# Optimization experiments

Hardware: AMD Instinct MI355X
Metric: run time of the kernel (lower is better)

Reference implementation:

```python
import jax, jax.numpy as jnp
import numpy as np

N = 100000   # neuron_count (nodes)
D = 128      # node feature dim
E = 2000000  # edges
NW = 8       # number of distinct weight matrices


def setup_inputs() -> dict:
    key = jax.random.key(0)
    k1, k2, k3, k4, k5 = jax.random.split(key, 5)
    x = jax.random.normal(k1, (N, D), dtype=jnp.float32)
    W = jax.random.normal(k2, (NW, D, D), dtype=jnp.float32) * 0.02
    u = jax.random.randint(k3, (E,), 0, N)      # edge source nodes
    v = jax.random.randint(k4, (E,), 0, N)      # edge dest nodes
    widx = jax.random.randint(k5, (E,), 0, NW)  # per-edge weight index
    return {"x": x, "W": W, "u": u, "v": v, "widx": widx}


def reference(x, W, u, v, widx):
    # DGL update_all: per-edge message m_e = W[widx_e] @ x[u_e], then
    # x_out[v] = tanh(sum of incoming m). Because the message is linear in
    # x_src, we aggregate source features per (weight-index, dest-node)
    # segment first, then apply each weight matrix once (grouped GEMM):
    #   out[v, i] = tanh( sum_w sum_j W[w, i, j] * S[w, v, j] )
    seg = widx * N + v                                   # combined segment id
    S = jax.ops.segment_sum(x[u], seg, num_segments=NW * N)  # [NW*N, D]
    S = S.reshape(NW, N, D)
    out = jnp.einsum("wij,wvj->vi", W, S)                # [N, D]
    # zero in-degree nodes: DGL gives 0 feature; tanh(0)=0, consistent.
    return jnp.tanh(out)
```

## Files before the change

### kernel.cpp

```cpp
#include <hip/hip_runtime.h>
#include <math.h>

#define D 128

typedef __attribute__((ext_vector_type(8))) short bf8;
typedef __attribute__((ext_vector_type(4))) float f32x4;

__device__ __forceinline__ unsigned short f2bf_rne(float f) {
  unsigned u = __float_as_uint(f);
  unsigned r = (u + 0x7FFFu + ((u >> 16) & 1u)) >> 16;
  return (unsigned short)r;
}
__device__ __forceinline__ float bf2f(unsigned short h) {
  return __uint_as_float(((unsigned)h) << 16);
}
__device__ __forceinline__ float bflo(unsigned p) {
  return __uint_as_float(p << 16);
}
__device__ __forceinline__ float bfhi(unsigned p) {
  return __uint_as_float(p & 0xFFFF0000u);
}

__global__ __launch_bounds__(256) void prep_kernel(
    const float* __restrict__ x, unsigned short* __restrict__ xbf,
    long long xTotal, int xcGrid,
    const int* __restrict__ v, const int* __restrict__ widx,
    int* __restrict__ cnt2, int* __restrict__ rank,
    long long E, long long N) {
  if (blockIdx.x < (unsigned)xcGrid) {
    long long i0 = ((long long)blockIdx.x * 256 + threadIdx.x) * 8;
    if (i0 + 8 > xTotal) return;
    float4 f0 = *(const float4*)(x + i0);
    float4 f1 = *(const float4*)(x + i0 + 4);
    unsigned short o[8];
    o[0] = f2bf_rne(f0.x); o[1] = f2bf_rne(f0.y);
    o[2] = f2bf_rne(f0.z); o[3] = f2bf_rne(f0.w);
    o[4] = f2bf_rne(f1.x); o[5] = f2bf_rne(f1.y);
    o[6] = f2bf_rne(f1.z); o[7] = f2bf_rne(f1.w);
    *(bf8*)(xbf + i0) = *(bf8*)o;
  } else {
    long long base = (long long)(blockIdx.x - xcGrid) * 1024;
    #pragma unroll
    for (int k = 0; k < 4; ++k) {
      long long e = base + k * 256 + threadIdx.x;
      if (e < E) {
        long long seg = (long long)widx[e] * N + v[e];
        rank[e] = atomicAdd(&cnt2[seg], 1);
      }
    }
  }
}

__global__ __launch_bounds__(1024) void scanA_kernel(
    const int* __restrict__ cnt2, int* __restrict__ starts2,
    int* __restrict__ blkSums, long long NB2) {
  __shared__ int part[1024];
  int tid = threadIdx.x;
  long long base = (long long)blockIdx.x * 4096 + tid * 4;
  int c[4];
  #pragma unroll
  for (int i = 0; i < 4; ++i)
    c[i] = (base + i < NB2) ? cnt2[base + i] : 0;
  int loc[4];
  int sum = 0;
  #pragma unroll
  for (int i = 0; i < 4; ++i) { loc[i] = sum; sum += c[i]; }
  part[tid] = sum;
  __syncthreads();
  for (int off = 1; off < 1024; off <<= 1) {
    int val = (tid >= off) ? part[tid - off] : 0;
    __syncthreads();
    part[tid] += val;
    __syncthreads();
  }
  int excl = (tid == 0) ? 0 : part[tid - 1];
  #pragma unroll
  for (int i = 0; i < 4; ++i)
    if (base + i < NB2) starts2[base + i] = excl + loc[i];
  if (tid == 1023) blkSums[blockIdx.x] = part[1023];
}

__global__ __launch_bounds__(1024) void scanC_kernel(
    int* __restrict__ starts2, const int* __restrict__ blkSums,
    long long NB2, int Etot, int nBlk) {
  __shared__ int part[256];
  int tid = threadIdx.x;
  if (tid < 256) part[tid] = (tid < nBlk) ? blkSums[tid] : 0;
  __syncthreads();
  for (int off = 1; off < 256; off <<= 1) {
    int val = 0;
    if (tid < 256 && tid >= off) val = part[tid - off];
    __syncthreads();
    if (tid < 256) part[tid] += val;
    __syncthreads();
  }
  int off = (blockIdx.x == 0) ? 0 : part[blockIdx.x - 1];
  long long base = (long long)blockIdx.x * 4096 + tid * 4;
  #pragma unroll
  for (int i = 0; i < 4; ++i) {
    long long idx = base + i;
    if (idx < NB2) starts2[idx] += off;
  }
  if (blockIdx.x == 0 && tid == 0) starts2[NB2] = Etot;
}

__global__ __launch_bounds__(256) void scatwc_kernel(
    const float* __restrict__ W, unsigned short* __restrict__ Wp, int NW,
    int wpGrid,
    const int* __restrict__ u, const int* __restrict__ v,
    const int* __restrict__ widx, const int* __restrict__ rank,
    const int* __restrict__ starts2, int* __restrict__ sortedU,
    long long E, long long N) {
  if (blockIdx.x < (unsigned)wpGrid) {
    int idx = blockIdx.x * 256 + threadIdx.x;
    if (idx >= NW * 2048) return;
    int lane = idx & 63;
    int ks = (idx >> 6) & 3;
    int n  = (idx >> 8) & 7;
    int w  = idx >> 11;
    int row = n * 16 + (lane & 15);
    int col = ks * 32 + (lane >> 4) * 8;
    const float* src = W + (size_t)w * D * D + (size_t)row * D + col;
    unsigned short hi[8], re[8];
    #pragma unroll
    for (int e = 0; e < 8; ++e) {
      float f = src[e];
      unsigned short h = f2bf_rne(f);
      hi[e] = h;
      re[e] = f2bf_rne(f - bf2f(h));
    }
    int frag = (w * 8 + n) * 4 + ks;
    unsigned short* dst = Wp + (size_t)frag * 1024 + lane * 8;
    *(bf8*)dst = *(bf8*)hi;
    *(bf8*)(dst + 512) = *(bf8*)re;
  } else {
    long long base = (long long)(blockIdx.x - wpGrid) * 1024;
    #pragma unroll
    for (int k = 0; k < 4; ++k) {
      long long e = base + k * 256 + threadIdx.x;
      if (e < E) {
        long long seg = (long long)widx[e] * N + v[e];
        int pos = starts2[seg] + rank[e];
        sortedU[pos] = u[e] * 32;
      }
    }
  }
}

__global__ __launch_bounds__(256) void gather_pack_kernel(
    const unsigned short* __restrict__ xbf, const int* __restrict__ starts2,
    const int* __restrict__ sortedU, unsigned short* __restrict__ Sp,
    long long N, long long nt16) {
  __shared__ float T[16][132];
  int tid = threadIdx.x;
  long long w = blockIdx.y;
  long long rt = blockIdx.x;
  long long r0 = rt * 16;
  int grp = tid >> 5;
  int lane = tid & 31;

  #pragma unroll
  for (int rr = 0; rr < 2; ++rr) {
    int rloc = grp + rr * 8;
    long long r = r0 + rloc;
    float ax = 0.f, ay = 0.f, az = 0.f, aw = 0.f;
    if (r < N) {
      long long seg = w * N + r;
      int s0 = starts2[seg];
      int s1 = starts2[seg + 1];
      const uint2* xb = (const uint2*)xbf;
      int i = s0;
      for (; i + 4 <= s1; i += 4) {
        int u0 = sortedU[i], u1 = sortedU[i + 1];
        int u2 = sortedU[i + 2], u3 = sortedU[i + 3];
        uint2 a0 = xb[(size_t)u0 + lane];
        uint2 a1 = xb[(size_t)u1 + lane];
        uint2 a2 = xb[(size_t)u2 + lane];
        uint2 a3 = xb[(size_t)u3 + lane];
        ax += (bflo(a0.x) + bflo(a1.x)) + (bflo(a2.x) + bflo(a3.x));
        ay += (bfhi(a0.x) + bfhi(a1.x)) + (bfhi(a2.x) + bfhi(a3.x));
        az += (bflo(a0.y) + bflo(a1.y)) + (bflo(a2.y) + bflo(a3.y));
        aw += (bfhi(a0.y) + bfhi(a1.y)) + (bfhi(a2.y) + bfhi(a3.y));
      }
      for (; i < s1; ++i) {
        int uu = sortedU[i];
        uint2 a = xb[(size_t)uu + lane];
        ax += bflo(a.x); ay += bfhi(a.x);
        az += bflo(a.y); aw += bfhi(a.y);
      }
    }
    *(float4*)&T[rloc][lane * 4] = make_float4(ax, ay, az, aw);
  }
  __syncthreads();

  int ks = tid >> 6;
  int l = tid & 63;
  const float* src = &T[l & 15][ks * 32 + (l >> 4) * 8];
  unsigned short o[8];
  #pragma unroll
  for (int e = 0; e < 8; ++e) o[e] = f2bf_rne(src[e]);
  size_t frag = ((size_t)w * nt16 + rt) * 4 + ks;
  *(bf8*)(Sp + frag * 512 + (size_t)l * 8) = *(bf8*)o;
}

template<int NWT>
__global__ __launch_bounds__(256, 3) void mfma_gemm_kernel(
    const unsigned short* __restrict__ Sp, const unsigned short* __restrict__ Wp,
    float* __restrict__ out, long long N, long long nt16, int NWdyn) {
  int tid = threadIdx.x;
  int wv = tid >> 6;
  int wr = wv >> 1;
  int wc = wv & 1;
  int l = tid & 63;
  long long rtBase = (long long)blockIdx.x * 4 + wr * 2;

  const unsigned short* SA = Sp + (size_t)rtBase * 2048 + (size_t)l * 8;
  const unsigned short* WB = Wp + (size_t)wc * 16384 + (size_t)l * 8;
  const size_t wStrideS = (size_t)nt16 * 2048;

  f32x4 acc[2][4];
  #pragma unroll
  for (int m = 0; m < 2; ++m)
    #pragma unroll
    for (int n = 0; n < 4; ++n) acc[m][n] = (f32x4)(0.f);

  if (NWT == 8) {
    bf8 a[4][2], bh[2][4], br[2][4];
    {
      a[0][0] = *(const bf8*)(SA);
      a[0][1] = *(const bf8*)(SA + 2048);
      a[1][0] = *(const bf8*)(SA + 512);
      a[1][1] = *(const bf8*)(SA + 512 + 2048);
      a[2][0] = *(const bf8*)(SA + 1024);
      a[2][1] = *(const bf8*)(SA + 1024 + 2048);
      #pragma unroll
      for (int n = 0; n < 4; ++n) {
        bh[0][n] = *(const bf8*)(WB + n * 4096);
        br[0][n] = *(const bf8*)(WB + n * 4096 + 512);
      }
    }
    #pragma unroll
    for (int s = 0; s < 32; ++s) {
      const int abuf = s & 3;
      const int bbuf = s & 1;
      if (s + 3 < 32) {
        const int t = s + 3, w2 = t >> 2, ks2 = t & 3;
        const unsigned short* sa = SA + (size_t)w2 * wStrideS + ks2 * 512;
        a[(s + 3) & 3][0] = *(const bf8*)(sa);
        a[(s + 3) & 3][1] = *(const bf8*)(sa + 2048);
      }
      if (s + 1 < 32) {
        const int t = s + 1, w2 = t >> 2, ks2 = t & 3;
        const unsigned short* wb = WB + (size_t)w2 * 32768 + ks2 * 1024;
        #pragma unroll
        for (int n = 0; n < 4; ++n) {
          bh[bbuf ^ 1][n] = *(const bf8*)(wb + n * 4096);
          br[bbuf ^ 1][n] = *(const bf8*)(wb + n * 4096 + 512);
        }
      }
      #pragma unroll
      for (int n = 0; n < 4; ++n)
        #pragma unroll
        for (int m = 0; m < 2; ++m) {
          acc[m][n] = __builtin_amdgcn_mfma_f32_16x16x32_bf16(a[abuf][m], bh[bbuf][n], acc[m][n], 0, 0, 0);
          acc[m][n] = __builtin_amdgcn_mfma_f32_16x16x32_bf16(a[abuf][m], br[bbuf][n], acc[m][n], 0, 0, 0);
        }
    }
  } else {
    for (int w = 0; w < NWdyn; ++w) {
      #pragma unroll
      for (int ks = 0; ks < 4; ++ks) {
        const unsigned short* sa = SA + (size_t)w * wStrideS + ks * 512;
        bf8 a0 = *(const bf8*)(sa);
        bf8 a1 = *(const bf8*)(sa + 2048);
        const unsigned short* wb = WB + (size_t)w * 32768 + ks * 1024;
        #pragma unroll
        for (int n = 0; n < 4; ++n) {
          bf8 bh0 = *(const bf8*)(wb + n * 4096);
          bf8 br0 = *(const bf8*)(wb + n * 4096 + 512);
          acc[0][n] = __builtin_amdgcn_mfma_f32_16x16x32_bf16(a0, bh0, acc[0][n], 0, 0, 0);
          acc[1][n] = __builtin_amdgcn_mfma_f32_16x16x32_bf16(a1, bh0, acc[1][n], 0, 0, 0);
          acc[0][n] = __builtin_amdgcn_mfma_f32_16x16x32_bf16(a0, br0, acc[0][n], 0, 0, 0);
          acc[1][n] = __builtin_amdgcn_mfma_f32_16x16x32_bf16(a1, br0, acc[1][n], 0, 0, 0);
        }
      }
    }
  }

  int lrow = l & 15;
  int crow0 = (l >> 4) * 4;
  #pragma unroll
  for (int m = 0; m < 2; ++m) {
    long long vbase = (rtBase + m) * 16 + crow0;
    #pragma unroll
    for (int rr = 0; rr < 4; ++rr) {
      long long v = vbase + rr;
      if (v < N) {
        float* op = out + v * D + wc * 64 + lrow;
        #pragma unroll
        for (int n = 0; n < 4; ++n) op[n * 16] = tanhf(acc[m][n][rr]);
      }
    }
  }
}

extern "C" void kernel_launch(void* const* d_in, const int* in_sizes, int n_in,
                              void* d_out, int out_size, void* d_ws, size_t ws_size,
                              hipStream_t stream) {
  const float* x    = (const float*)d_in[0];
  const float* W    = (const float*)d_in[1];
  const int*   u    = (const int*)d_in[2];
  const int*   v    = (const int*)d_in[3];
  const int*   widx = (const int*)d_in[4];

  long long N  = (long long)in_sizes[0] / D;
  int       NW = in_sizes[1] / (D * D);
  long long E  = (long long)in_sizes[2];
  float* out = (float*)d_out;

  long long NB2 = (long long)NW * N;
  int gemmBlocks = (int)((N + 63) / 64);
  long long NpadA = (long long)gemmBlocks * 64;
  long long nt16 = NpadA / 16;
  int nScanBlk = (int)((NB2 + 4095) / 4096);
  long long xTotal = N * D;

  char* ws = (char*)d_ws;
  int* cnt2    = (int*)ws;                        ws += (size_t)NB2 * sizeof(int);
  int* starts2 = (int*)ws;                        ws += ((size_t)NB2 + 1) * sizeof(int);
  int* rank    = (int*)ws;                        ws += (size_t)E * sizeof(int);
  int* blkSums = (int*)ws;                        ws += 256 * sizeof(int);
  int* sortedU = (int*)ws;                        ws += (size_t)E * sizeof(int);
  ws = (char*)(((uintptr_t)ws + 255) & ~(uintptr_t)255);
  unsigned short* Wp = (unsigned short*)ws;       ws += (size_t)NW * 32768 * 2;
  ws = (char*)(((uintptr_t)ws + 255) & ~(uintptr_t)255);
  unsigned short* xbf = (unsigned short*)ws;      ws += (size_t)xTotal * 2;
  ws = (char*)(((uintptr_t)ws + 255) & ~(uintptr_t)255);
  unsigned short* Sp = (unsigned short*)ws;       ws += (size_t)NW * NpadA * D * 2;
  (void)ws_size;

  dim3 blk(256);
  int edgeGrid4 = (int)((E + 1023) / 1024);
  int wpGrid = (NW * 2048 + 255) / 256;
  int xcGrid = (int)((xTotal / 8 + 255) / 256);

  hipMemsetAsync(cnt2, 0, (size_t)NB2 * sizeof(int), stream);
  prep_kernel<<<xcGrid + edgeGrid4, blk, 0, stream>>>(
      x, xbf, xTotal, xcGrid, v, widx, cnt2, rank, E, N);
  scanA_kernel<<<nScanBlk, 1024, 0, stream>>>(cnt2, starts2, blkSums, NB2);
  scanC_kernel<<<nScanBlk, 1024, 0, stream>>>(starts2, blkSums, NB2,
                                              (int)E, nScanBlk);
  scatwc_kernel<<<wpGrid + edgeGrid4, blk, 0, stream>>>(
      W, Wp, NW, wpGrid, u, v, widx, rank, starts2, sortedU, E, N);
  dim3 ggrid((unsigned)nt16, (unsigned)NW);
  gather_pack_kernel<<<ggrid, blk, 0, stream>>>(xbf, starts2, sortedU, Sp, N, nt16);
  if (NW == 8) {
    mfma_gemm_kernel<8><<<gemmBlocks, blk, 0, stream>>>(
        Sp, Wp, out, N, nt16, NW);
  } else {
    mfma_gemm_kernel<0><<<gemmBlocks, blk, 0, stream>>>(
        Sp, Wp, out, N, nt16, NW);
  }
}
```

Measured before the change: 421.0 us.

## Balance gather work across block by edge ranges with LDS atomic accumulation

```diff
diff --git a/kernel.cpp b/kernel.cpp
--- a/kernel.cpp
+++ b/kernel.cpp
@@ -139,9 +139,10 @@
     for (int k = 0; k < 4; ++k) {
       long long e = base + k * 256 + threadIdx.x;
       if (e < E) {
-        long long seg = (long long)widx[e] * N + v[e];
+        int vv = v[e];
+        long long seg = (long long)widx[e] * N + vv;
         int pos = starts2[seg] + rank[e];
-        sortedU[pos] = u[e] * 32;
+        sortedU[pos] = u[e] * 32 | (vv & 15);
       }
     }
   }
@@ -151,54 +152,63 @@
     const unsigned short* __restrict__ xbf, const int* __restrict__ starts2,
     const int* __restrict__ sortedU, unsigned short* __restrict__ Sp,
     long long N, long long nt16) {
-  __shared__ float T[16][132];
+  __shared__ float Sc[4][16][32];
   int tid = threadIdx.x;
   long long w = blockIdx.y;
   long long rt = blockIdx.x;
-  long long r0 = rt * 16;
   int grp = tid >> 5;
   int lane = tid & 31;
 
-  #pragma unroll
-  for (int rr = 0; rr < 2; ++rr) {
-    int rloc = grp + rr * 8;
-    long long r = r0 + rloc;
-    float ax = 0.f, ay = 0.f, az = 0.f, aw = 0.f;
-    if (r < N) {
-      long long seg = w * N + r;
-      int s0 = starts2[seg];
-      int s1 = starts2[seg + 1];
-      const uint2* xb = (const uint2*)xbf;
-      int i = s0;
-      for (; i + 4 <= s1; i += 4) {
-        int u0 = sortedU[i], u1 = sortedU[i + 1];
-        int u2 = sortedU[i + 2], u3 = sortedU[i + 3];
-        uint2 a0 = xb[(size_t)u0 + lane];
-        uint2 a1 = xb[(size_t)u1 + lane];
-        uint2 a2 = xb[(size_t)u2 + lane];
-        uint2 a3 = xb[(size_t)u3 + lane];
-        ax += (bflo(a0.x) + bflo(a1.x)) + (bflo(a2.x) + bflo(a3.x));
-        ay += (bfhi(a0.x) + bfhi(a1.x)) + (bfhi(a2.x) + bfhi(a3.x));
-        az += (bflo(a0.y) + bflo(a1.y)) + (bflo(a2.y) + bflo(a3.y));
-        aw += (bfhi(a0.y) + bfhi(a1.y)) + (bfhi(a2.y) + bfhi(a3.y));
-      }
-      for (; i < s1; ++i) {
-        int uu = sortedU[i];
-        uint2 a = xb[(size_t)uu + lane];
-        ax += bflo(a.x); ay += bfhi(a.x);
-        az += bflo(a.y); aw += bfhi(a.y);
-      }
-    }
-    *(float4*)&T[rloc][lane * 4] = make_float4(ax, ay, az, aw);
+  {
+    float4* z = (float4*)&Sc[0][0][0];
+    z[tid] = make_float4(0.f, 0.f, 0.f, 0.f);
+    z[tid + 256] = make_float4(0.f, 0.f, 0.f, 0.f);
+  }
+  __syncthreads();
+
+  long long rlo = rt * 16; if (rlo > N) rlo = N;
+  long long rhi = rt * 16 + 16; if (rhi > N) rhi = N;
+  int s0 = starts2[w * N + rlo];
+  int s1 = starts2[w * N + rhi];
+
+  const uint2* xb = (const uint2*)xbf;
+  for (int i = s0 + grp; i < s1; i += 32) {
+    unsigned rec[4];
+    uint2 av[4];
+    #pragma unroll
+    for (int k = 0; k < 4; ++k) {
+      int j = i + k * 8;
+      if (j < s1) rec[k] = (unsigned)sortedU[j];
+    }
+    #pragma unroll
+    for (int k = 0; k < 4; ++k) {
+      int j = i + k * 8;
+      if (j < s1) av[k] = xb[(size_t)(rec[k] & 0xFFFFFFE0u) + lane];
+    }
+    #pragma unroll
+    for (int k = 0; k < 4; ++k) {
+      int j = i + k * 8;
+      if (j < s1) {
+        int vl = rec[k] & 15;
+        atomicAdd(&Sc[0][vl][lane], bflo(av[k].x));
+        atomicAdd(&Sc[1][vl][lane], bfhi(av[k].x));
+        atomicAdd(&Sc[2][vl][lane], bflo(av[k].y));
+        atomicAdd(&Sc[3][vl][lane], bfhi(av[k].y));
+      }
+    }
   }
   __syncthreads();
 
   int ks = tid >> 6;
   int l = tid & 63;
-  const float* src = &T[l & 15][ks * 32 + (l >> 4) * 8];
+  int row = l & 15;
+  int colbase = ks * 32 + (l >> 4) * 8;
   unsigned short o[8];
   #pragma unroll
-  for (int e = 0; e < 8; ++e) o[e] = f2bf_rne(src[e]);
+  for (int e = 0; e < 8; ++e) {
+    int col = colbase + e;
+    o[e] = f2bf_rne(Sc[col & 3][row][col >> 2]);
+  }
   size_t frag = ((size_t)w * nt16 + rt) * 4 + ks;
   *(bf8*)(Sp + frag * 512 + (size_t)l * 8) = *(bf8*)o;
 }
```

Measured after the change: 1.649 ms. +291.8%, slower.
